# Performance work log

Hardware: AMD Instinct MI355X
Metric: run time of the kernel (lower is better)

The kernel has to match this reference:

```python
import jax, jax.numpy as jnp
import numpy as np
import math

D_MODEL = 1024
N_HEADS = 16
D_K = 64
D_V = 64
B = 4
S = 1024


def setup_inputs() -> dict:
    key = jax.random.key(0)
    ks = jax.random.split(key, 11)
    # xavier-ish init scale for projections
    s_in = 1.0 / math.sqrt(D_MODEL)
    return {
        "queries": jax.random.normal(ks[0], (B, S, D_MODEL), jnp.float32),
        "keys": jax.random.normal(ks[1], (B, S, D_MODEL), jnp.float32),
        "values": jax.random.normal(ks[2], (B, S, D_MODEL), jnp.float32),
        "Wq": jax.random.normal(ks[3], (D_MODEL, N_HEADS * D_K), jnp.float32) * s_in,
        "bq": jnp.zeros((N_HEADS * D_K,), jnp.float32),
        "Wk": jax.random.normal(ks[4], (D_MODEL, N_HEADS * D_K), jnp.float32) * s_in,
        "bk": jnp.zeros((N_HEADS * D_K,), jnp.float32),
        "Wv": jax.random.normal(ks[5], (D_MODEL, N_HEADS * D_V), jnp.float32) * s_in,
        "bv": jnp.zeros((N_HEADS * D_V,), jnp.float32),
        "Wo": jax.random.normal(ks[6], (N_HEADS * D_V, D_MODEL), jnp.float32) * (1.0 / math.sqrt(N_HEADS * D_V)),
        "bo": jnp.zeros((D_MODEL,), jnp.float32),
    }


def reference(queries, keys, values, Wq, bq, Wk, bk, Wv, bv, Wo, bo):
    Bq, Sq, _ = queries.shape
    Sk = keys.shape[1]
    scale = 1.0 / math.sqrt(D_K)
    # projections -> [B, S, H, d]
    q = (queries @ Wq + bq).reshape(Bq, Sq, N_HEADS, D_K)
    k = (keys @ Wk + bk).reshape(Bq, Sk, N_HEADS, D_K)
    v = (values @ Wv + bv).reshape(Bq, Sk, N_HEADS, D_V)
    # scaled dot-product attention: scores [B, H, Sq, Sk]
    scores = jnp.einsum("bqhd,bkhd->bhqk", q, k) * scale
    attn = jax.nn.softmax(scores, axis=-1)
    # weighted values -> [B, Sq, H*D_V]
    out = jnp.einsum("bhqk,bkhd->bqhd", attn, v).reshape(Bq, Sq, N_HEADS * D_V)
    return out @ Wo + bo
```

## Files before the change

### kernel.cpp

```cpp
#include <hip/hip_runtime.h>
#include <hip/hip_bf16.h>

typedef __attribute__((ext_vector_type(4))) float f32x4;
typedef __attribute__((ext_vector_type(16))) float f32x16;
typedef __attribute__((ext_vector_type(8))) short bf16x8;
typedef __attribute__((ext_vector_type(4))) unsigned short u16x4;
typedef __attribute__((ext_vector_type(8))) unsigned short u16x8;
typedef __attribute__((ext_vector_type(2))) unsigned int u32x2;

#define MFMA16(a, b, c) __builtin_amdgcn_mfma_f32_16x16x32_bf16((a), (b), (c), 0, 0, 0)
#define MFMA32(a, b, c) __builtin_amdgcn_mfma_f32_32x32x16_bf16((a), (b), (c), 0, 0, 0)

static __device__ __forceinline__ unsigned short f2bf(float f) {
    union { float f; unsigned int u; } v; v.f = f;
    unsigned int r = v.u + 0x7FFFu + ((v.u >> 16) & 1u);
    return (unsigned short)(r >> 16);
}
static __device__ __forceinline__ unsigned int pk2(float x, float y) {
    unsigned int r;
    asm("v_cvt_pk_bf16_f32 %0, %1, %2" : "=v"(r) : "v"(x), "v"(y));
    return r;
}
static __device__ __forceinline__ float bf2f(unsigned short u) {
    return __uint_as_float((unsigned int)u << 16);
}

static __device__ __forceinline__ void gload_lds16(const void* g, void* l) {
    __builtin_amdgcn_global_load_lds(
        (const __attribute__((address_space(1))) void*)g,
        (__attribute__((address_space(3))) void*)l, 16, 0, 0);
}

__global__ __launch_bounds__(256) void prepass(
    const float* __restrict__ q, const float* __restrict__ k,
    const float* __restrict__ v, const float* __restrict__ Wq,
    const float* __restrict__ Wk, const float* __restrict__ Wv,
    const float* __restrict__ Wo, unsigned short* __restrict__ qc,
    unsigned short* __restrict__ kc, unsigned short* __restrict__ vc,
    unsigned short* __restrict__ Wt, unsigned short* __restrict__ Wot) {
    __shared__ unsigned short T[64][65];
    const int id = blockIdx.x, t = threadIdx.x;
    if (id < 6144) {
        const int z = id >> 11;
        const float* src = z == 0 ? q : (z == 1 ? k : v);
        unsigned short* dst = z == 0 ? qc : (z == 1 ? kc : vc);
        size_t off = ((size_t)(id & 2047) * 256 + t) * 8;
        f32x4 a = *(const f32x4*)&src[off];
        f32x4 b = *(const f32x4*)&src[off + 4];
        union { unsigned int u[4]; u16x8 v; } o;
        o.u[0] = pk2(a[0], a[1]); o.u[1] = pk2(a[2], a[3]);
        o.u[2] = pk2(b[0], b[1]); o.u[3] = pk2(b[2], b[3]);
        *(u16x8*)&dst[off] = o.v;
    } else {
        int r = id - 6144;
        const int z = r >> 8; r &= 255;
        const float* W = z == 0 ? Wq : (z == 1 ? Wk : (z == 2 ? Wv : Wo));
        unsigned short* Wd = z < 3 ? (Wt + (size_t)z * 1024 * 1024) : Wot;
        const int k0 = (r >> 4) * 64, n0 = (r & 15) * 64;
        const int rl = t >> 4, c4 = (t & 15) * 4;
#pragma unroll
        for (int i = 0; i < 4; ++i) {
            f32x4 vv = *(const f32x4*)&W[(size_t)(k0 + rl + 16 * i) * 1024 + n0 + c4];
#pragma unroll
            for (int j = 0; j < 4; ++j) T[rl + 16 * i][c4 + j] = f2bf(vv[j]);
        }
        __syncthreads();
#pragma unroll
        for (int i = 0; i < 4; ++i) {
            u16x4 o;
#pragma unroll
            for (int j = 0; j < 4; ++j) o[j] = T[c4 + j][rl + 16 * i];
            *(u16x4*)&Wd[(size_t)(n0 + rl + 16 * i) * 1024 + k0 + c4] = o;
        }
    }
}

template <bool OUT_BF16, int BM>
__global__ __launch_bounds__(256, 2) void gemm_fast(
    const unsigned short* __restrict__ A0, const unsigned short* __restrict__ A1,
    const unsigned short* __restrict__ A2, const unsigned short* __restrict__ Wt,
    const float* __restrict__ b0, const float* __restrict__ b1,
    const float* __restrict__ b2, void* __restrict__ Outv, int ldo) {
    constexpr int MF = BM / 32;
    __shared__ __align__(16) unsigned short As[2][BM * 32];
    __shared__ __align__(16) unsigned short Bs[2][128 * 32];

    const int t = threadIdx.x;
    const int w = t >> 6, lane = t & 63;
    const int wr = w >> 1, wc = w & 1;
    const int g = lane >> 4, r15 = lane & 15;
    const int bm = blockIdx.y * BM;
    const int bn = blockIdx.x * 128;
    const int msel = bn >> 10;
    const unsigned short* A = msel == 0 ? A0 : (msel == 1 ? A1 : A2);
    const float* bias = msel == 0 ? b0 : (msel == 1 ? b1 : b2);
    const int l4 = lane >> 2, c8 = (lane & 3) * 8;

    f32x4 acc[MF][4];
#pragma unroll
    for (int m = 0; m < MF; ++m)
#pragma unroll
        for (int n = 0; n < 4; ++n) acc[m][n] = (f32x4){0.f, 0.f, 0.f, 0.f};

#define G_STAGE(BUF, KT)                                                          \
    {                                                                             \
        gload_lds16(&A[(size_t)(bm + 16 * w + l4) * 1024 + (KT) + c8],            \
                    &As[BUF][w * 512]);                                           \
        if (BM == 128)                                                            \
            gload_lds16(&A[(size_t)(bm + 16 * (w + 4) + l4) * 1024 + (KT) + c8],  \
                        &As[BUF][((w + 4) * 512) % (BM * 32)]);                   \
        gload_lds16(&Wt[(size_t)(bn + 16 * w + l4) * 1024 + (KT) + c8],           \
                    &Bs[BUF][w * 512]);                                           \
        gload_lds16(&Wt[(size_t)(bn + 16 * (w + 4) + l4) * 1024 + (KT) + c8],     \
                    &Bs[BUF][(w + 4) * 512]);                                     \
    }

    G_STAGE(0, 0);
    __syncthreads();

    int cur = 0;
    for (int kt = 0; kt < 1024; kt += 32) {
        if (kt < 992) G_STAGE(cur ^ 1, kt + 32);
        bf16x8 af[MF], bfr[4];
#pragma unroll
        for (int m = 0; m < MF; ++m)
            af[m] = *(const bf16x8*)&As[cur][(wr * (BM / 2) + m * 16 + r15) * 32 + g * 8];
#pragma unroll
        for (int n = 0; n < 4; ++n)
            bfr[n] = *(const bf16x8*)&Bs[cur][(wc * 64 + n * 16 + r15) * 32 + g * 8];
        __builtin_amdgcn_s_setprio(1);
#pragma unroll
        for (int m = 0; m < MF; ++m)
#pragma unroll
            for (int n = 0; n < 4; ++n)
                acc[m][n] = MFMA16(af[m], bfr[n], acc[m][n]);
        __builtin_amdgcn_s_setprio(0);
        __syncthreads();
        cur ^= 1;
    }
#undef G_STAGE

    float* Of = (float*)Outv;
    unsigned short* Ob = (unsigned short*)Outv;
#pragma unroll
    for (int n = 0; n < 4; ++n) {
        int col = bn + wc * 64 + n * 16 + r15;
        float bv = bias[col & 1023];
#pragma unroll
        for (int m = 0; m < MF; ++m) {
#pragma unroll
            for (int r = 0; r < 4; ++r) {
                int row = bm + wr * (BM / 2) + m * 16 + g * 4 + r;
                float val = acc[m][n][r] + bv;
                if (OUT_BF16)
                    Ob[(size_t)row * ldo + col] = f2bf(val);
                else
                    Of[(size_t)row * ldo + col] = val;
            }
        }
    }
}

__global__ __launch_bounds__(256, 4) void attn32_kernel(
    const unsigned short* __restrict__ Q, const unsigned short* __restrict__ K,
    const unsigned short* __restrict__ V, unsigned short* __restrict__ Opart,
    float* __restrict__ ML, int ld) {
    __shared__ __align__(16) unsigned short Kls[2][64 * 80];
    __shared__ __align__(16) unsigned short Vls[2][64 * 80];

    const int t = threadIdx.x;
    const int w = t >> 6, lane = t & 63;
    const int q5 = lane & 31, hi = lane >> 5;

    const int id = blockIdx.x;
    const int sid = (id & 7) * 128 + (id >> 3);
    const int bh = sid >> 4, sub = sid & 15;
    const int qb = sub >> 1, half = sub & 1;
    const int b = bh >> 4, h = bh & 15;
    const int brow = b * 1024;
    const int q0 = qb * 128;
    const int kv0 = half * 512;

    const float c2 = 0.18033688f;

    const unsigned short* Qrow = Q + (size_t)(brow + q0 + w * 32 + q5) * ld + h * 64;
    bf16x8 qreg[8];
#pragma unroll
    for (int j = 0; j < 8; ++j) qreg[j] = *(const bf16x8*)&Qrow[8 * j];
    bf16x8 qsel[4];
#pragma unroll
    for (int kk = 0; kk < 4; ++kk) qsel[kk] = hi ? qreg[2 * kk + 1] : qreg[2 * kk];

    const int krow = t >> 2, kpart = t & 3;
    const int vp = t & 31, vdc = t >> 5;
    const unsigned short* Kg = K + h * 64;
    const unsigned short* Vg = V + h * 64;

    u16x8 kr0, kr1, vr0, vr1;
#define STG_LOAD(KT)                                                            \
    {                                                                           \
        size_t kro = (size_t)(brow + (KT) + krow) * ld;                         \
        kr0 = *(const u16x8*)&Kg[kro + kpart * 8];                              \
        kr1 = *(const u16x8*)&Kg[kro + kpart * 8 + 32];                         \
        size_t vro = (size_t)(brow + (KT) + 2 * vp) * ld;                       \
        vr0 = *(const u16x8*)&Vg[vro + vdc * 8];                                \
        vr1 = *(const u16x8*)&Vg[vro + ld + vdc * 8];                           \
    }
#define STG_WRITE(BUF)                                                          \
    {                                                                           \
        char* kb_ = (char*)Kls[BUF];                                            \
        int tg_ = (krow & 7) << 4;                                              \
        *(u16x8*)(kb_ + krow * 160 + ((kpart * 16) ^ tg_)) = kr0;               \
        *(u16x8*)(kb_ + krow * 160 + (((kpart + 4) * 16) ^ tg_)) = kr1;         \
        char* vb_ = (char*)Vls[BUF];                                            \
        _Pragma("unroll") for (int j_ = 0; j_ < 8; ++j_) {                      \
            int d_ = vdc * 8 + j_;                                              \
            unsigned int pk_ = (unsigned int)(unsigned short)vr0[j_] |          \
                               ((unsigned int)(unsigned short)vr1[j_] << 16);   \
            *(unsigned int*)(vb_ + d_ * 160 + ((vp * 4) ^ ((d_ & 7) << 4)))     \
                = pk_;                                                          \
        }                                                                       \
    }

    f32x16 acc0 = {}, acc1 = {};
    float mrun = -1e30f, lrun = 0.f;

    STG_LOAD(kv0);
    STG_WRITE(0);
    __syncthreads();

    int cur = 0;
    for (int tile = 0; tile < 8; ++tile) {
        const bool more = tile < 7;
        if (more) STG_LOAD(kv0 + tile * 64 + 64);

        char* kb = (char*)Kls[cur];
        f32x16 st0 = {}, st1 = {};
        {
            const int tg0 = (q5 & 7) << 4;
            char* kp0 = kb + q5 * 160;
            char* kp1 = kb + (q5 + 32) * 160;
            __builtin_amdgcn_s_setprio(1);
#pragma unroll
            for (int kk = 0; kk < 4; ++kk) {
                int so = ((2 * kk + hi) * 16) ^ tg0;
                bf16x8 kf0 = *(const bf16x8*)(kp0 + so);
                bf16x8 kf1 = *(const bf16x8*)(kp1 + so);
                st0 = MFMA32(kf0, qsel[kk], st0);
                st1 = MFMA32(kf1, qsel[kk], st1);
            }
            __builtin_amdgcn_s_setprio(0);
        }

        float mloc = fmaxf(st0[0], st0[1]);
#pragma unroll
        for (int r = 2; r < 16; ++r) mloc = fmaxf(mloc, st0[r]);
#pragma unroll
        for (int r = 0; r < 16; ++r) mloc = fmaxf(mloc, st1[r]);
        mloc = fmaxf(mloc, __shfl_xor(mloc, 32));
        if (!__all(mloc - mrun <= 64.f)) {
            float mnew = fmaxf(mrun, mloc);
            float sf = exp2f((mrun - mnew) * c2);
            mrun = mnew;
            lrun *= sf;
#pragma unroll
            for (int r = 0; r < 16; ++r) { acc0[r] *= sf; acc1[r] *= sf; }
        }
        float mneg = -mrun * c2;
        float rs = 0.f;
#pragma unroll
        for (int r = 0; r < 16; ++r) {
            st0[r] = exp2f(fmaf(st0[r], c2, mneg));
            rs += st0[r];
        }
#pragma unroll
        for (int r = 0; r < 16; ++r) {
            st1[r] = exp2f(fmaf(st1[r], c2, mneg));
            rs += st1[r];
        }
        rs += __shfl_xor(rs, 32);
        lrun += rs;

        char* vb = (char*)Vls[cur];
        const int tgv = (q5 & 7) << 4;
        char* vp0 = vb + q5 * 160;
        char* vp1 = vb + (q5 + 32) * 160;
        __builtin_amdgcn_s_setprio(1);
#define PV_HALF(ST, CT)                                                         \
    _Pragma("unroll") for (int ks = 0; ks < 2; ++ks) {                          \
        unsigned int a0 = pk2(ST[8 * ks + 0], ST[8 * ks + 1]);                  \
        unsigned int a1 = pk2(ST[8 * ks + 2], ST[8 * ks + 3]);                  \
        unsigned int a2 = pk2(ST[8 * ks + 4], ST[8 * ks + 5]);                  \
        unsigned int a3 = pk2(ST[8 * ks + 6], ST[8 * ks + 7]);                  \
        unsigned int x0 = __shfl_xor(a0, 32), x1 = __shfl_xor(a1, 32);          \
        unsigned int x2 = __shfl_xor(a2, 32), x3 = __shfl_xor(a3, 32);          \
        union { unsigned int u[4]; bf16x8 v; } pfu;                             \
        pfu.u[0] = hi ? x2 : a0;                                                \
        pfu.u[1] = hi ? x3 : a1;                                                \
        pfu.u[2] = hi ? a2 : x0;                                                \
        pfu.u[3] = hi ? a3 : x1;                                                \
        int co = ((32 * (2 * (CT) + ks) + 16 * hi)) ^ tgv;                      \
        bf16x8 vf0 = *(const bf16x8*)(vp0 + co);                                \
        bf16x8 vf1 = *(const bf16x8*)(vp1 + co);                                \
        acc0 = MFMA32(vf0, pfu.v, acc0);                                        \
        acc1 = MFMA32(vf1, pfu.v, acc1);                                        \
    }
        PV_HALF(st0, 0);
        PV_HALF(st1, 1);
        __builtin_amdgcn_s_setprio(0);

        if (more) STG_WRITE(cur ^ 1);
        __syncthreads();
        cur ^= 1;
    }

    const int grow = brow + q0 + w * 32 + q5;
    const float inv = 1.0f / lrun;
    unsigned short* Orow =
        Opart + (size_t)half * 4194304 + (size_t)grow * 1024 + h * 64;
#pragma unroll
    for (int k = 0; k < 4; ++k) {
        int d0 = 8 * k + 4 * hi;
        u32x2 pa, pb;
        pa[0] = pk2(acc0[4 * k + 0] * inv, acc0[4 * k + 1] * inv);
        pa[1] = pk2(acc0[4 * k + 2] * inv, acc0[4 * k + 3] * inv);
        *(u32x2*)&Orow[d0] = pa;
        pb[0] = pk2(acc1[4 * k + 0] * inv, acc1[4 * k + 1] * inv);
        pb[1] = pk2(acc1[4 * k + 2] * inv, acc1[4 * k + 3] * inv);
        *(u32x2*)&Orow[32 + d0] = pb;
    }
    if (hi == 0)
        ((float2*)ML)[half * 65536 + grow * 16 + h] = make_float2(mrun, lrun);
#undef STG_LOAD
#undef STG_WRITE
#undef PV_HALF
}

__global__ __launch_bounds__(256) void attn_merge(
    const unsigned short* __restrict__ Opart, const float* __restrict__ ML,
    unsigned short* __restrict__ Omg) {
    const float c2 = 0.18033688f;
    const int gid = blockIdx.x * 256 + threadIdx.x;
    const int pair = gid >> 3;
    const int dp = gid & 7;
    const int row = pair >> 4, h = pair & 15;
    const float2 ml0 = ((const float2*)ML)[pair];
    const float2 ml1 = ((const float2*)ML)[65536 + pair];
    float mn = fmaxf(ml0.x, ml1.x);
    float w0 = ml0.y * exp2f((ml0.x - mn) * c2);
    float w1 = ml1.y * exp2f((ml1.x - mn) * c2);
    float inv = 1.0f / (w0 + w1);
    w0 *= inv; w1 *= inv;
    size_t off = (size_t)row * 1024 + h * 64 + dp * 8;
    u16x8 a = *(const u16x8*)&Opart[off];
    u16x8 b = *(const u16x8*)&Opart[4194304 + off];
    union { unsigned int u[4]; u16x8 v; } o;
#pragma unroll
    for (int j = 0; j < 4; ++j)
        o.u[j] = pk2(bf2f(a[2 * j]) * w0 + bf2f(b[2 * j]) * w1,
                     bf2f(a[2 * j + 1]) * w0 + bf2f(b[2 * j + 1]) * w1);
    *(u16x8*)&Omg[off] = o.v;
}

extern "C" void kernel_launch(void* const* d_in, const int* in_sizes, int n_in,
                              void* d_out, int out_size, void* d_ws, size_t ws_size,
                              hipStream_t stream) {
    const float* q  = (const float*)d_in[0];
    const float* k  = (const float*)d_in[1];
    const float* v  = (const float*)d_in[2];
    const float* Wq = (const float*)d_in[3];
    const float* bq = (const float*)d_in[4];
    const float* Wk = (const float*)d_in[5];
    const float* bk = (const float*)d_in[6];
    const float* Wv = (const float*)d_in[7];
    const float* bv = (const float*)d_in[8];
    const float* Wo = (const float*)d_in[9];
    const float* bo = (const float*)d_in[10];

    const size_t M1 = (size_t)1024 * 1024;
    unsigned short* qc  = (unsigned short*)d_ws;
    unsigned short* kc  = qc + 4 * M1;
    unsigned short* vc  = kc + 4 * M1;
    unsigned short* Wt  = vc + 4 * M1;
    unsigned short* Wot = Wt + 3 * M1;
    unsigned short* QKV = Wot + M1;
    unsigned short* Opart = qc;
    float* ML = (float*)vc;
    unsigned short* Omg = QKV;

    dim3 bt(256, 1, 1);
    prepass<<<dim3(7168), bt, 0, stream>>>(q, k, v, Wq, Wk, Wv, Wo,
                                           qc, kc, vc, Wt, Wot);
    gemm_fast<true, 128><<<dim3(24, 32), bt, 0, stream>>>(
        qc, kc, vc, Wt, bq, bk, bv, QKV, 3072);
    attn32_kernel<<<dim3(1024), bt, 0, stream>>>(
        QKV, QKV + 1024, QKV + 2048, Opart, ML, 3072);
    attn_merge<<<dim3(2048), bt, 0, stream>>>(Opart, ML, Omg);
    gemm_fast<false, 64><<<dim3(8, 64), bt, 0, stream>>>(
        Omg, Omg, Omg, Wot, bo, bo, bo, d_out, 1024);
}
```

Before: 232.9 us.

## Drop split-KV attention and merge pass; add XCD-aware GEMM tile swizzle

The attention kernel no longer splits the KV range in two. Each block now walks all 16 KV tiles and writes the normalized bf16 output directly, which removes the partial-output and ML buffers and the separate merge kernel. The GEMMs switch to a 1D grid with an XCD-aware block-to-tile mapping meant to improve L2 locality. The output GEMM now uses 64x64 tiles with a 1024-block grid and min-waves 4. The attention grid halves to 512 blocks with launch bounds lowered to 2, which reduces parallelism but saves a launch and an extra memory round trip.

```diff
diff --git a/kernel.cpp b/kernel.cpp
--- a/kernel.cpp
+++ b/kernel.cpp
@@ -20,9 +20,6 @@
     unsigned int r;
     asm("v_cvt_pk_bf16_f32 %0, %1, %2" : "=v"(r) : "v"(x), "v"(y));
     return r;
-}
-static __device__ __forceinline__ float bf2f(unsigned short u) {
-    return __uint_as_float((unsigned int)u << 16);
 }
 
 static __device__ __forceinline__ void gload_lds16(const void* g, void* l) {
@@ -75,32 +72,46 @@
     }
 }
 
-template <bool OUT_BF16, int BM>
-__global__ __launch_bounds__(256, 2) void gemm_fast(
+template <bool OUT_BF16, int BM, int BN, int SWZ, int MINW>
+__global__ __launch_bounds__(256, MINW) void gemm_fast(
     const unsigned short* __restrict__ A0, const unsigned short* __restrict__ A1,
     const unsigned short* __restrict__ A2, const unsigned short* __restrict__ Wt,
     const float* __restrict__ b0, const float* __restrict__ b1,
     const float* __restrict__ b2, void* __restrict__ Outv, int ldo) {
     constexpr int MF = BM / 32;
+    constexpr int NF = BN / 32;
     __shared__ __align__(16) unsigned short As[2][BM * 32];
-    __shared__ __align__(16) unsigned short Bs[2][128 * 32];
+    __shared__ __align__(16) unsigned short Bs[2][BN * 32];
 
     const int t = threadIdx.x;
     const int w = t >> 6, lane = t & 63;
     const int wr = w >> 1, wc = w & 1;
     const int g = lane >> 4, r15 = lane & 15;
-    const int bm = blockIdx.y * BM;
-    const int bn = blockIdx.x * 128;
+
+    const int id = blockIdx.x;
+    int bm, bn;
+    if (SWZ == 0) {
+        const int xcd = id & 7, local = id >> 3;
+        const int half = local >= 48 ? 1 : 0;
+        const int ww = local - half * 48;
+        const int gg = xcd * 2 + half;
+        bm = ((gg >> 2) * 8 + (ww & 7)) * BM;
+        bn = ((gg & 3) * 6 + (ww >> 3)) * BN;
+    } else {
+        const int xcd = id & 7, local = id >> 3;
+        bm = (xcd * 8 + (local & 7)) * BM;
+        bn = (local >> 3) * BN;
+    }
     const int msel = bn >> 10;
     const unsigned short* A = msel == 0 ? A0 : (msel == 1 ? A1 : A2);
     const float* bias = msel == 0 ? b0 : (msel == 1 ? b1 : b2);
     const int l4 = lane >> 2, c8 = (lane & 3) * 8;
 
-    f32x4 acc[MF][4];
+    f32x4 acc[MF][NF];
 #pragma unroll
     for (int m = 0; m < MF; ++m)
 #pragma unroll
-        for (int n = 0; n < 4; ++n) acc[m][n] = (f32x4){0.f, 0.f, 0.f, 0.f};
+        for (int n = 0; n < NF; ++n) acc[m][n] = (f32x4){0.f, 0.f, 0.f, 0.f};
 
 #define G_STAGE(BUF, KT)                                                          \
     {                                                                             \
@@ -108,11 +119,12 @@
                     &As[BUF][w * 512]);                                           \
         if (BM == 128)                                                            \
             gload_lds16(&A[(size_t)(bm + 16 * (w + 4) + l4) * 1024 + (KT) + c8],  \
-                        &As[BUF][((w + 4) * 512) % (BM * 32)]);                   \
+                        &As[BUF][(w + 4) * 512]);                                 \
         gload_lds16(&Wt[(size_t)(bn + 16 * w + l4) * 1024 + (KT) + c8],           \
                     &Bs[BUF][w * 512]);                                           \
-        gload_lds16(&Wt[(size_t)(bn + 16 * (w + 4) + l4) * 1024 + (KT) + c8],     \
-                    &Bs[BUF][(w + 4) * 512]);                                     \
+        if (BN == 128)                                                            \
+            gload_lds16(&Wt[(size_t)(bn + 16 * (w + 4) + l4) * 1024 + (KT) + c8], \
+                        &Bs[BUF][(w + 4) * 512]);                                 \
     }
 
     G_STAGE(0, 0);
@@ -121,18 +133,18 @@
     int cur = 0;
     for (int kt = 0; kt < 1024; kt += 32) {
         if (kt < 992) G_STAGE(cur ^ 1, kt + 32);
-        bf16x8 af[MF], bfr[4];
+        bf16x8 af[MF], bfr[NF];
 #pragma unroll
         for (int m = 0; m < MF; ++m)
             af[m] = *(const bf16x8*)&As[cur][(wr * (BM / 2) + m * 16 + r15) * 32 + g * 8];
 #pragma unroll
-        for (int n = 0; n < 4; ++n)
-            bfr[n] = *(const bf16x8*)&Bs[cur][(wc * 64 + n * 16 + r15) * 32 + g * 8];
+        for (int n = 0; n < NF; ++n)
+            bfr[n] = *(const bf16x8*)&Bs[cur][(wc * (BN / 2) + n * 16 + r15) * 32 + g * 8];
         __builtin_amdgcn_s_setprio(1);
 #pragma unroll
         for (int m = 0; m < MF; ++m)
 #pragma unroll
-            for (int n = 0; n < 4; ++n)
+            for (int n = 0; n < NF; ++n)
                 acc[m][n] = MFMA16(af[m], bfr[n], acc[m][n]);
         __builtin_amdgcn_s_setprio(0);
         __syncthreads();
@@ -143,8 +155,8 @@
     float* Of = (float*)Outv;
     unsigned short* Ob = (unsigned short*)Outv;
 #pragma unroll
-    for (int n = 0; n < 4; ++n) {
-        int col = bn + wc * 64 + n * 16 + r15;
+    for (int n = 0; n < NF; ++n) {
+        int col = bn + wc * (BN / 2) + n * 16 + r15;
         float bv = bias[col & 1023];
 #pragma unroll
         for (int m = 0; m < MF; ++m) {
@@ -161,10 +173,9 @@
     }
 }
 
-__global__ __launch_bounds__(256, 4) void attn32_kernel(
+__global__ __launch_bounds__(256, 2) void attn32_kernel(
     const unsigned short* __restrict__ Q, const unsigned short* __restrict__ K,
-    const unsigned short* __restrict__ V, unsigned short* __restrict__ Opart,
-    float* __restrict__ ML, int ld) {
+    const unsigned short* __restrict__ V, unsigned short* __restrict__ O, int ld) {
     __shared__ __align__(16) unsigned short Kls[2][64 * 80];
     __shared__ __align__(16) unsigned short Vls[2][64 * 80];
 
@@ -173,13 +184,11 @@
     const int q5 = lane & 31, hi = lane >> 5;
 
     const int id = blockIdx.x;
-    const int sid = (id & 7) * 128 + (id >> 3);
-    const int bh = sid >> 4, sub = sid & 15;
-    const int qb = sub >> 1, half = sub & 1;
+    const int sid = (id & 7) * 64 + (id >> 3);
+    const int bh = sid >> 3, qb = sid & 7;
     const int b = bh >> 4, h = bh & 15;
     const int brow = b * 1024;
     const int q0 = qb * 128;
-    const int kv0 = half * 512;
 
     const float c2 = 0.18033688f;
 
@@ -225,14 +234,14 @@
     f32x16 acc0 = {}, acc1 = {};
     float mrun = -1e30f, lrun = 0.f;
 
-    STG_LOAD(kv0);
+    STG_LOAD(0);
     STG_WRITE(0);
     __syncthreads();
 
     int cur = 0;
-    for (int tile = 0; tile < 8; ++tile) {
-        const bool more = tile < 7;
-        if (more) STG_LOAD(kv0 + tile * 64 + 64);
+    for (int tile = 0; tile < 16; ++tile) {
+        const bool more = tile < 15;
+        if (more) STG_LOAD(tile * 64 + 64);
 
         char* kb = (char*)Kls[cur];
         f32x16 st0 = {}, st1 = {};
@@ -314,10 +323,8 @@
         cur ^= 1;
     }
 
-    const int grow = brow + q0 + w * 32 + q5;
     const float inv = 1.0f / lrun;
-    unsigned short* Orow =
-        Opart + (size_t)half * 4194304 + (size_t)grow * 1024 + h * 64;
+    unsigned short* Orow = O + (size_t)(brow + q0 + w * 32 + q5) * 1024 + h * 64;
 #pragma unroll
     for (int k = 0; k < 4; ++k) {
         int d0 = 8 * k + 4 * hi;
@@ -329,37 +336,9 @@
         pb[1] = pk2(acc1[4 * k + 2] * inv, acc1[4 * k + 3] * inv);
         *(u32x2*)&Orow[32 + d0] = pb;
     }
-    if (hi == 0)
-        ((float2*)ML)[half * 65536 + grow * 16 + h] = make_float2(mrun, lrun);
 #undef STG_LOAD
 #undef STG_WRITE
 #undef PV_HALF
-}
-
-__global__ __launch_bounds__(256) void attn_merge(
-    const unsigned short* __restrict__ Opart, const float* __restrict__ ML,
-    unsigned short* __restrict__ Omg) {
-    const float c2 = 0.18033688f;
-    const int gid = blockIdx.x * 256 + threadIdx.x;
-    const int pair = gid >> 3;
-    const int dp = gid & 7;
-    const int row = pair >> 4, h = pair & 15;
-    const float2 ml0 = ((const float2*)ML)[pair];
-    const float2 ml1 = ((const float2*)ML)[65536 + pair];
-    float mn = fmaxf(ml0.x, ml1.x);
-    float w0 = ml0.y * exp2f((ml0.x - mn) * c2);
-    float w1 = ml1.y * exp2f((ml1.x - mn) * c2);
-    float inv = 1.0f / (w0 + w1);
-    w0 *= inv; w1 *= inv;
-    size_t off = (size_t)row * 1024 + h * 64 + dp * 8;
-    u16x8 a = *(const u16x8*)&Opart[off];
-    u16x8 b = *(const u16x8*)&Opart[4194304 + off];
-    union { unsigned int u[4]; u16x8 v; } o;
-#pragma unroll
-    for (int j = 0; j < 4; ++j)
-        o.u[j] = pk2(bf2f(a[2 * j]) * w0 + bf2f(b[2 * j]) * w1,
-                     bf2f(a[2 * j + 1]) * w0 + bf2f(b[2 * j + 1]) * w1);
-    *(u16x8*)&Omg[off] = o.v;
 }
 
 extern "C" void kernel_launch(void* const* d_in, const int* in_sizes, int n_in,
@@ -384,18 +363,15 @@
     unsigned short* Wt  = vc + 4 * M1;
     unsigned short* Wot = Wt + 3 * M1;
     unsigned short* QKV = Wot + M1;
-    unsigned short* Opart = qc;
-    float* ML = (float*)vc;
-    unsigned short* Omg = QKV;
+    unsigned short* Ob  = qc;
 
     dim3 bt(256, 1, 1);
     prepass<<<dim3(7168), bt, 0, stream>>>(q, k, v, Wq, Wk, Wv, Wo,
                                            qc, kc, vc, Wt, Wot);
-    gemm_fast<true, 128><<<dim3(24, 32), bt, 0, stream>>>(
+    gemm_fast<true, 128, 128, 0, 2><<<dim3(768), bt, 0, stream>>>(
         qc, kc, vc, Wt, bq, bk, bv, QKV, 3072);
-    attn32_kernel<<<dim3(1024), bt, 0, stream>>>(
-        QKV, QKV + 1024, QKV + 2048, Opart, ML, 3072);
-    attn_merge<<<dim3(2048), bt, 0, stream>>>(Opart, ML, Omg);
-    gemm_fast<false, 64><<<dim3(8, 64), bt, 0, stream>>>(
-        Omg, Omg, Omg, Wot, bo, bo, bo, d_out, 1024);
-}
+    attn32_kernel<<<dim3(512), bt, 0, stream>>>(
+        QKV, QKV + 1024, QKV + 2048, Ob, 3072);
+    gemm_fast<false, 64, 64, 1, 4><<<dim3(1024), bt, 0, stream>>>(
+        Ob, Ob, Ob, Wot, bo, bo, bo, d_out, 1024);
+}
```

Measured after the change: 211.9 us. 1.1x faster.

## Remap GEMM tiles per XCD for L2 locality and retile output projection

Applied to the files above, without the earlier changes.

The GEMM kernel now takes a 1D grid and remaps block IDs so that blocks landing on the same XCD (id&7) work on neighbouring M/N tiles, which should improve L2 reuse of A and W panels. The output projection switches from 64x128 to 128x64 tiles, with a swizzle that gives each XCD its own band of rows. The attention kernel's launch bounds drop from 4 to 2 waves-per-SIMD minimum, which frees registers but may lower occupancy. The remap hardcodes the grid sizes (768 and 512 blocks), so it is tied to these shapes.

```diff
diff --git a/kernel.cpp b/kernel.cpp
--- a/kernel.cpp
+++ b/kernel.cpp
@@ -75,32 +75,47 @@
     }
 }
 
-template <bool OUT_BF16, int BM>
-__global__ __launch_bounds__(256, 2) void gemm_fast(
+template <bool OUT_BF16, int BM, int BN, int SWZ, int MINW>
+__global__ __launch_bounds__(256, MINW) void gemm_fast(
     const unsigned short* __restrict__ A0, const unsigned short* __restrict__ A1,
     const unsigned short* __restrict__ A2, const unsigned short* __restrict__ Wt,
     const float* __restrict__ b0, const float* __restrict__ b1,
     const float* __restrict__ b2, void* __restrict__ Outv, int ldo) {
     constexpr int MF = BM / 32;
+    constexpr int NF = BN / 32;
     __shared__ __align__(16) unsigned short As[2][BM * 32];
-    __shared__ __align__(16) unsigned short Bs[2][128 * 32];
+    __shared__ __align__(16) unsigned short Bs[2][BN * 32];
 
     const int t = threadIdx.x;
     const int w = t >> 6, lane = t & 63;
     const int wr = w >> 1, wc = w & 1;
     const int g = lane >> 4, r15 = lane & 15;
-    const int bm = blockIdx.y * BM;
-    const int bn = blockIdx.x * 128;
+
+    const int id = blockIdx.x;
+    int bm, bn;
+    if (SWZ == 0) {
+        const int xcd = id & 7, local = id >> 3;
+        const int half = local >= 48 ? 1 : 0;
+        const int ww = local - half * 48;
+        const int gg = xcd * 2 + half;
+        bm = ((gg >> 2) * 8 + (ww & 7)) * BM;
+        bn = ((gg & 3) * 6 + (ww >> 3)) * BN;
+    } else {
+        constexpr int MPX = (4096 / BM) / 8;
+        const int xcd = id & 7, local = id >> 3;
+        bm = (xcd * MPX + (local % MPX)) * BM;
+        bn = (local / MPX) * BN;
+    }
     const int msel = bn >> 10;
     const unsigned short* A = msel == 0 ? A0 : (msel == 1 ? A1 : A2);
     const float* bias = msel == 0 ? b0 : (msel == 1 ? b1 : b2);
     const int l4 = lane >> 2, c8 = (lane & 3) * 8;
 
-    f32x4 acc[MF][4];
+    f32x4 acc[MF][NF];
 #pragma unroll
     for (int m = 0; m < MF; ++m)
 #pragma unroll
-        for (int n = 0; n < 4; ++n) acc[m][n] = (f32x4){0.f, 0.f, 0.f, 0.f};
+        for (int n = 0; n < NF; ++n) acc[m][n] = (f32x4){0.f, 0.f, 0.f, 0.f};
 
 #define G_STAGE(BUF, KT)                                                          \
     {                                                                             \
@@ -108,11 +123,12 @@
                     &As[BUF][w * 512]);                                           \
         if (BM == 128)                                                            \
             gload_lds16(&A[(size_t)(bm + 16 * (w + 4) + l4) * 1024 + (KT) + c8],  \
-                        &As[BUF][((w + 4) * 512) % (BM * 32)]);                   \
+                        &As[BUF][(w + 4) * 512]);                                 \
         gload_lds16(&Wt[(size_t)(bn + 16 * w + l4) * 1024 + (KT) + c8],           \
-                    &Bs[BUF][w * 512]);                                           \
-        gload_lds16(&Wt[(size_t)(bn + 16 * (w + 4) + l4) * 1024 + (KT) + c8],     \
-                    &Bs[BUF][(w + 4) * 512]);                                     \
+                    &Bs[BUF][(w * 512) % (BN * 32)]);                             \
+        if (BN == 128)                                                            \
+            gload_lds16(&Wt[(size_t)(bn + 16 * (w + 4) + l4) * 1024 + (KT) + c8], \
+                        &Bs[BUF][((w + 4) * 512) % (BN * 32)]);                   \
     }
 
     G_STAGE(0, 0);
@@ -121,18 +137,18 @@
     int cur = 0;
     for (int kt = 0; kt < 1024; kt += 32) {
         if (kt < 992) G_STAGE(cur ^ 1, kt + 32);
-        bf16x8 af[MF], bfr[4];
+        bf16x8 af[MF], bfr[NF];
 #pragma unroll
         for (int m = 0; m < MF; ++m)
             af[m] = *(const bf16x8*)&As[cur][(wr * (BM / 2) + m * 16 + r15) * 32 + g * 8];
 #pragma unroll
-        for (int n = 0; n < 4; ++n)
-            bfr[n] = *(const bf16x8*)&Bs[cur][(wc * 64 + n * 16 + r15) * 32 + g * 8];
+        for (int n = 0; n < NF; ++n)
+            bfr[n] = *(const bf16x8*)&Bs[cur][(wc * (BN / 2) + n * 16 + r15) * 32 + g * 8];
         __builtin_amdgcn_s_setprio(1);
 #pragma unroll
         for (int m = 0; m < MF; ++m)
 #pragma unroll
-            for (int n = 0; n < 4; ++n)
+            for (int n = 0; n < NF; ++n)
                 acc[m][n] = MFMA16(af[m], bfr[n], acc[m][n]);
         __builtin_amdgcn_s_setprio(0);
         __syncthreads();
@@ -143,8 +159,8 @@
     float* Of = (float*)Outv;
     unsigned short* Ob = (unsigned short*)Outv;
 #pragma unroll
-    for (int n = 0; n < 4; ++n) {
-        int col = bn + wc * 64 + n * 16 + r15;
+    for (int n = 0; n < NF; ++n) {
+        int col = bn + wc * (BN / 2) + n * 16 + r15;
         float bv = bias[col & 1023];
 #pragma unroll
         for (int m = 0; m < MF; ++m) {
@@ -161,7 +177,7 @@
     }
 }
 
-__global__ __launch_bounds__(256, 4) void attn32_kernel(
+__global__ __launch_bounds__(256, 2) void attn32_kernel(
     const unsigned short* __restrict__ Q, const unsigned short* __restrict__ K,
     const unsigned short* __restrict__ V, unsigned short* __restrict__ Opart,
     float* __restrict__ ML, int ld) {
@@ -391,11 +407,11 @@
     dim3 bt(256, 1, 1);
     prepass<<<dim3(7168), bt, 0, stream>>>(q, k, v, Wq, Wk, Wv, Wo,
                                            qc, kc, vc, Wt, Wot);
-    gemm_fast<true, 128><<<dim3(24, 32), bt, 0, stream>>>(
+    gemm_fast<true, 128, 128, 0, 2><<<dim3(768), bt, 0, stream>>>(
         qc, kc, vc, Wt, bq, bk, bv, QKV, 3072);
     attn32_kernel<<<dim3(1024), bt, 0, stream>>>(
         QKV, QKV + 1024, QKV + 2048, Opart, ML, 3072);
     attn_merge<<<dim3(2048), bt, 0, stream>>>(Opart, ML, Omg);
-    gemm_fast<false, 64><<<dim3(8, 64), bt, 0, stream>>>(
+    gemm_fast<false, 128, 64, 1, 2><<<dim3(512), bt, 0, stream>>>(
         Omg, Omg, Omg, Wot, bo, bo, bo, d_out, 1024);
 }
```

New measurement: 218.7 us. 1.07x faster.
